# Performance work log

Hardware: AMD Instinct MI355X
Metric: run time of the kernel (lower is better)

The kernel has to match this reference:

```python
import jax, jax.numpy as jnp
import numpy as np

TANH_CLIP = 10.0
TEMP = 1.0


def setup_inputs() -> dict:
    key = jax.random.key(0)
    ks = jax.random.split(key, 8)
    B, N, E, H, SC = 1024, 1000, 128, 8, 256
    dk = E // H
    context = jax.random.normal(ks[0], (B, 1, E), dtype=jnp.float32)
    step_context = jax.random.normal(ks[1], (B, 1, SC), dtype=jnp.float32)
    # scale weights so tanh/softmax stay in a sane numeric range
    W_step = jax.random.normal(ks[2], (E, SC), dtype=jnp.float32) * 0.05
    glimpse_K = jax.random.normal(ks[3], (H, B, 1, N, dk), dtype=jnp.float32)
    glimpse_V = jax.random.normal(ks[4], (H, B, 1, N, dk), dtype=jnp.float32)
    logit_K = jax.random.normal(ks[5], (B, 1, N, E), dtype=jnp.float32)
    W_out = jax.random.normal(ks[6], (E, E), dtype=jnp.float32) * 0.05
    mask = jax.random.randint(ks[7], (B, 1, N), 0, 2).astype(bool)
    mask = mask.at[:, :, 0].set(False)  # guarantee at least one feasible node
    return {"context": context, "step_context": step_context, "W_step": W_step,
            "glimpse_K": glimpse_K, "glimpse_V": glimpse_V, "logit_K": logit_K,
            "W_out": W_out, "mask": mask}


def reference(context, step_context, W_step, glimpse_K, glimpse_V, logit_K, W_out, mask):
    B, S, E = context.shape          # S = num_steps = 1
    H = glimpse_K.shape[0]
    dk = E // H
    neg_inf = jnp.float32(-jnp.inf)
    # query = context_node_projected + project_step_context(step_context)
    query = context + jnp.einsum('bsc,ec->bse', step_context, W_step)  # [B,S,E]
    # split heads: glimpse_Q -> [H,B,S,dk] (the singleton q-dim of the torch code is folded)
    Q = query.reshape(B, S, H, dk).transpose(2, 0, 1, 3)
    # compatibility [H,B,S,N]
    compat = jnp.einsum('hbsk,hbsnk->hbsn', Q, glimpse_K) / jnp.sqrt(jnp.float32(dk))
    compat = jnp.where(mask[None], neg_inf, compat)       # mask_inner
    attn = jax.nn.softmax(compat, axis=-1)
    heads = jnp.einsum('hbsn,hbsnk->hbsk', attn, glimpse_V)  # [H,B,S,dk]
    glimpse = heads.transpose(1, 2, 0, 3).reshape(B, S, E)   # concat heads
    glimpse = jnp.einsum('bse,oe->bso', glimpse, W_out)      # project_out
    # logits against logit_K  [B,S,N]
    logits = jnp.einsum('bse,bsne->bsn', glimpse, logit_K) / jnp.sqrt(jnp.float32(E))
    logits = jnp.tanh(logits) * jnp.float32(TANH_CLIP)       # tanh clipping
    logits = jnp.where(mask, neg_inf, logits)                # mask_logits
    log_p = jax.nn.log_softmax(logits / jnp.float32(TEMP), axis=-1)
    return log_p
```

## Files before the change

### kernel.cpp

```cpp
#include <hip/hip_runtime.h>
#include <hip/hip_bf16.h>
#include <math.h>

#define NB  1024
#define NN  1000
#define NE  128
#define NH  8
#define NDK 16
#define NSC 256

typedef __attribute__((ext_vector_type(4))) float f32x4;

__device__ __forceinline__ f32x4 ld4(const float* p) {
    return *reinterpret_cast<const f32x4*>(p);
}

__global__ __launch_bounds__(512, 4)
void fused_kernel(const float* __restrict__ ctx, const float* __restrict__ stepc,
                  const float* __restrict__ Wstep,
                  const float* __restrict__ gK, const float* __restrict__ gV,
                  const float* __restrict__ lK, const float* __restrict__ Wout,
                  const unsigned char* __restrict__ mask,
                  __hip_bfloat16* __restrict__ out)
{
    const int b = blockIdx.x;
    const int t = threadIdx.x;
    const int w = t >> 6, lane = t & 63;
    const int qq  = lane & 3;
    const int rsl = lane >> 2;

    __shared__ __align__(16) float q_lds[NE];
    __shared__ float wmax[2][8], wsum[2][8];
    __shared__ __align__(16) float wred[2][8][16];
    __shared__ __align__(16) float g[NE];
    __shared__ __align__(16) float gout[NE];
    __shared__ float red[8];
    __shared__ float Mv, LSv;

    const unsigned int* mw = reinterpret_cast<const unsigned int*>(mask);
    const bool m_i32 = (__ballot(mw[lane] <= 1u) == ~0ull);
    const int* mask_i = reinterpret_cast<const int*>(mask);

    {
        const f32x4 sv = ld4(stepc + (size_t)b * NSC + lane * 4);
        #pragma unroll
        for (int r = 0; r < 16; ++r) {
            const int row = w * NDK + r;
            f32x4 wv = ld4(Wstep + (size_t)row * NSC + lane * 4);
            float p = wv.x * sv.x + wv.y * sv.y + wv.z * sv.z + wv.w * sv.w;
            #pragma unroll
            for (int off = 32; off > 0; off >>= 1) p += __shfl_xor(p, off);
            if (lane == 0) q_lds[row] = p + ctx[(size_t)b * NE + row];
        }
    }

    unsigned mbits = 0;
    #pragma unroll
    for (int i = 0; i < 8; ++i) {
        const int n = w * 16 + i * 128 + rsl;
        const bool dead = (n >= NN);
        const int nn = dead ? 0 : n;
        int mk = m_i32 ? (mask_i[(size_t)b * NN + nn] != 0)
                       : (mask[(size_t)b * NN + nn] != 0);
        mbits |= (unsigned)(mk | (dead ? 1 : 0)) << i;
    }
    __syncthreads();

    #pragma unroll 1
    for (int h = 0; h < NH; ++h) {
        const int pb = h & 1;
        const f32x4 qv = ld4(&q_lds[h * NDK + qq * 4]);
        const float* Kb = gK + (size_t)(h * NB + b) * NN * NDK;
        const float* Vb = gV + (size_t)(h * NB + b) * NN * NDK;

        f32x4 vreg[8];
        float sc[8];
        #pragma unroll
        for (int i = 0; i < 8; ++i) {
            const int n = w * 16 + i * 128 + rsl;
            const int nn = (n < NN) ? n : 0;
            const size_t off = (size_t)nn * NDK + qq * 4;
            f32x4 kv = ld4(Kb + off);
            vreg[i] = ld4(Vb + off);
            sc[i] = kv.x*qv.x + kv.y*qv.y + kv.z*qv.z + kv.w*qv.w;
        }
        #pragma unroll
        for (int i = 0; i < 8; ++i) {
            float p = sc[i];
            p += __shfl_xor(p, 1);
            p += __shfl_xor(p, 2);
            sc[i] = ((mbits >> i) & 1u) ? -INFINITY : p * 0.25f;
        }

        float m = sc[0];
        #pragma unroll
        for (int i = 1; i < 8; ++i) m = fmaxf(m, sc[i]);
        #pragma unroll
        for (int off = 32; off > 0; off >>= 1) m = fmaxf(m, __shfl_xor(m, off));
        if (lane == 0) wmax[pb][w] = m;
        __syncthreads();
        float M = wmax[pb][0];
        #pragma unroll
        for (int i = 1; i < 8; ++i) M = fmaxf(M, wmax[pb][i]);

        f32x4 acc = {0.f, 0.f, 0.f, 0.f};
        float ls = 0.f;
        #pragma unroll
        for (int i = 0; i < 8; ++i) {
            const float e = expf(sc[i] - M);
            ls += e;
            acc.x += e * vreg[i].x; acc.y += e * vreg[i].y;
            acc.z += e * vreg[i].z; acc.w += e * vreg[i].w;
        }
        #pragma unroll
        for (int off = 32; off > 0; off >>= 1) ls += __shfl_xor(ls, off);
        if (lane == 0) wsum[pb][w] = ls;

        #pragma unroll
        for (int off = 4; off < 64; off <<= 1) {
            acc.x += __shfl_xor(acc.x, off);
            acc.y += __shfl_xor(acc.y, off);
            acc.z += __shfl_xor(acc.z, off);
            acc.w += __shfl_xor(acc.w, off);
        }
        if (lane < 4) *reinterpret_cast<f32x4*>(&wred[pb][w][lane * 4]) = acc;
        __syncthreads();

        if (t < NDK) {
            float S = wsum[pb][0];
            #pragma unroll
            for (int i = 1; i < 8; ++i) S += wsum[pb][i];
            S *= 0.25f;
            float r = wred[pb][0][t];
            #pragma unroll
            for (int i = 1; i < 8; ++i) r += wred[pb][i][t];
            g[h * NDK + t] = r / S;
        }
    }
    __syncthreads();

    if (t < NE) {
        float a2 = 0.f;
        const float4* w4 = reinterpret_cast<const float4*>(Wout + (size_t)t * NE);
        const float4* g4 = reinterpret_cast<const float4*>(g);
        #pragma unroll 8
        for (int e4 = 0; e4 < NE / 4; ++e4) {
            float4 wv = w4[e4]; float4 gg = g4[e4];
            a2 += wv.x*gg.x + wv.y*gg.y + wv.z*gg.z + wv.w*gg.w;
        }
        gout[t] = a2;
    }
    __syncthreads();

    const f32x4* go4 = reinterpret_cast<const f32x4*>(gout);
    float lv[2];
    #pragma unroll
    for (int i = 0; i < 2; ++i) {
        const int n = t + 512 * i;
        const bool live = (n < NN);
        const int nidx = live ? n : 0;
        int mkd = m_i32 ? (mask_i[(size_t)b * NN + nidx] != 0)
                        : (mask[(size_t)b * NN + nidx] != 0);
        mkd |= (live ? 0 : 1);
        const int nn = mkd ? 0 : n;
        const float* lp = lK + ((size_t)b * NN + nn) * NE;
        float a3 = 0.f;
        #pragma unroll
        for (int c4 = 0; c4 < NE / 4; ++c4) {
            f32x4 x = ld4(lp + 4 * c4);
            f32x4 gv = go4[c4];
            a3 += x.x*gv.x + x.y*gv.y + x.z*gv.z + x.w*gv.w;
        }
        float val = tanhf(a3 * 0.08838834764831845f) * 10.0f;
        lv[i] = mkd ? -3.0e38f : val;
    }

    float mm = fmaxf(lv[0], lv[1]);
    #pragma unroll
    for (int off = 32; off > 0; off >>= 1) mm = fmaxf(mm, __shfl_xor(mm, off));
    if (lane == 0) red[w] = mm;
    __syncthreads();
    if (t == 0) {
        float m2 = red[0];
        #pragma unroll
        for (int i = 1; i < 8; ++i) m2 = fmaxf(m2, red[i]);
        Mv = m2;
    }
    __syncthreads();
    const float M2 = Mv;
    float s2 = expf(lv[0] - M2) + expf(lv[1] - M2);
    #pragma unroll
    for (int off = 32; off > 0; off >>= 1) s2 += __shfl_xor(s2, off);
    if (lane == 0) red[w] = s2;
    __syncthreads();
    if (t == 0) {
        float ss = 0.f;
        #pragma unroll
        for (int i = 0; i < 8; ++i) ss += red[i];
        LSv = M2 + logf(ss);
    }
    __syncthreads();
    const float LS = LSv;
    #pragma unroll
    for (int i = 0; i < 2; ++i) {
        const int n = t + 512 * i;
        if (n < NN)
            out[(size_t)b * NN + n] = __float2bfloat16(lv[i] - LS);
    }
}

extern "C" void kernel_launch(void* const* d_in, const int* in_sizes, int n_in,
                              void* d_out, int out_size, void* d_ws, size_t ws_size,
                              hipStream_t stream) {
    const float* ctx   = (const float*)d_in[0];
    const float* stepc = (const float*)d_in[1];
    const float* Wstep = (const float*)d_in[2];
    const float* gK    = (const float*)d_in[3];
    const float* gV    = (const float*)d_in[4];
    const float* lK    = (const float*)d_in[5];
    const float* Wout  = (const float*)d_in[6];
    const unsigned char* mask = (const unsigned char*)d_in[7];
    __hip_bfloat16* out = (__hip_bfloat16*)d_out;

    fused_kernel<<<dim3(NB), dim3(512), 0, stream>>>(
        ctx, stepc, Wstep, gK, gV, lK, Wout, mask, out);
}
```

Baseline: 257.5 us.

## Assign one head per wave with online softmax over nodes

Each of the 8 waves now owns one attention head and streams all 1000 nodes itself, keeping a running max, sum and accumulator (online softmax) instead of splitting nodes across waves with per-head block barriers. The query slice is computed straight into registers, so the LDS staging and the two __syncthreads per head go away. Masked nodes are redirected to row 0 so their K/V loads hit a single cached line, and fast __expf replaces expf. In exchange each wave runs a long serial loop with a rescale step per node, and the K/V loads inside one wave are less spread across memory.

```diff
diff --git a/kernel.cpp b/kernel.cpp
--- a/kernel.cpp
+++ b/kernel.cpp
@@ -8,6 +8,7 @@
 #define NH  8
 #define NDK 16
 #define NSC 256
+#define NIT 63
 
 typedef __attribute__((ext_vector_type(4))) float f32x4;
 
@@ -29,9 +30,6 @@
     const int qq  = lane & 3;
     const int rsl = lane >> 2;
 
-    __shared__ __align__(16) float q_lds[NE];
-    __shared__ float wmax[2][8], wsum[2][8];
-    __shared__ __align__(16) float wred[2][8][16];
     __shared__ __align__(16) float g[NE];
     __shared__ __align__(16) float gout[NE];
     __shared__ float red[8];
@@ -41,101 +39,78 @@
     const bool m_i32 = (__ballot(mw[lane] <= 1u) == ~0ull);
     const int* mask_i = reinterpret_cast<const int*>(mask);
 
+    float qv0 = 0.f, qv1 = 0.f, qv2 = 0.f, qv3 = 0.f;
     {
         const f32x4 sv = ld4(stepc + (size_t)b * NSC + lane * 4);
         #pragma unroll
-        for (int r = 0; r < 16; ++r) {
-            const int row = w * NDK + r;
-            f32x4 wv = ld4(Wstep + (size_t)row * NSC + lane * 4);
-            float p = wv.x * sv.x + wv.y * sv.y + wv.z * sv.z + wv.w * sv.w;
+        for (int rr = 0; rr < 4; ++rr) {
             #pragma unroll
-            for (int off = 32; off > 0; off >>= 1) p += __shfl_xor(p, off);
-            if (lane == 0) q_lds[row] = p + ctx[(size_t)b * NE + row];
+            for (int c = 0; c < 4; ++c) {
+                const int row = w * NDK + rr * 4 + c;
+                f32x4 wv = ld4(Wstep + (size_t)row * NSC + lane * 4);
+                float p = wv.x*sv.x + wv.y*sv.y + wv.z*sv.z + wv.w*sv.w;
+                #pragma unroll
+                for (int off = 32; off > 0; off >>= 1) p += __shfl_xor(p, off);
+                const float val = p + ctx[(size_t)b * NE + row];
+                const bool sel = (qq == rr);
+                if      (c == 0) qv0 = sel ? val : qv0;
+                else if (c == 1) qv1 = sel ? val : qv1;
+                else if (c == 2) qv2 = sel ? val : qv2;
+                else             qv3 = sel ? val : qv3;
+            }
         }
     }
 
-    unsigned mbits = 0;
-    #pragma unroll
-    for (int i = 0; i < 8; ++i) {
-        const int n = w * 16 + i * 128 + rsl;
+    const float* Kb = gK + (size_t)(w * NB + b) * NN * NDK;
+    const float* Vb = gV + (size_t)(w * NB + b) * NN * NDK;
+    float m = -3.0e38f, ls = 0.f;
+    f32x4 acc = {0.f, 0.f, 0.f, 0.f};
+    #pragma unroll 4
+    for (int it = 0; it < NIT; ++it) {
+        const int n = it * 16 + rsl;
         const bool dead = (n >= NN);
-        const int nn = dead ? 0 : n;
-        int mk = m_i32 ? (mask_i[(size_t)b * NN + nn] != 0)
-                       : (mask[(size_t)b * NN + nn] != 0);
-        mbits |= (unsigned)(mk | (dead ? 1 : 0)) << i;
-    }
-    __syncthreads();
-
-    #pragma unroll 1
-    for (int h = 0; h < NH; ++h) {
-        const int pb = h & 1;
-        const f32x4 qv = ld4(&q_lds[h * NDK + qq * 4]);
-        const float* Kb = gK + (size_t)(h * NB + b) * NN * NDK;
-        const float* Vb = gV + (size_t)(h * NB + b) * NN * NDK;
-
-        f32x4 vreg[8];
-        float sc[8];
-        #pragma unroll
-        for (int i = 0; i < 8; ++i) {
-            const int n = w * 16 + i * 128 + rsl;
-            const int nn = (n < NN) ? n : 0;
-            const size_t off = (size_t)nn * NDK + qq * 4;
-            f32x4 kv = ld4(Kb + off);
-            vreg[i] = ld4(Vb + off);
-            sc[i] = kv.x*qv.x + kv.y*qv.y + kv.z*qv.z + kv.w*qv.w;
-        }
-        #pragma unroll
-        for (int i = 0; i < 8; ++i) {
-            float p = sc[i];
-            p += __shfl_xor(p, 1);
-            p += __shfl_xor(p, 2);
-            sc[i] = ((mbits >> i) & 1u) ? -INFINITY : p * 0.25f;
-        }
-
-        float m = sc[0];
-        #pragma unroll
-        for (int i = 1; i < 8; ++i) m = fmaxf(m, sc[i]);
-        #pragma unroll
-        for (int off = 32; off > 0; off >>= 1) m = fmaxf(m, __shfl_xor(m, off));
-        if (lane == 0) wmax[pb][w] = m;
-        __syncthreads();
-        float M = wmax[pb][0];
-        #pragma unroll
-        for (int i = 1; i < 8; ++i) M = fmaxf(M, wmax[pb][i]);
-
-        f32x4 acc = {0.f, 0.f, 0.f, 0.f};
-        float ls = 0.f;
-        #pragma unroll
-        for (int i = 0; i < 8; ++i) {
-            const float e = expf(sc[i] - M);
-            ls += e;
-            acc.x += e * vreg[i].x; acc.y += e * vreg[i].y;
-            acc.z += e * vreg[i].z; acc.w += e * vreg[i].w;
-        }
-        #pragma unroll
-        for (int off = 32; off > 0; off >>= 1) ls += __shfl_xor(ls, off);
-        if (lane == 0) wsum[pb][w] = ls;
-
-        #pragma unroll
-        for (int off = 4; off < 64; off <<= 1) {
-            acc.x += __shfl_xor(acc.x, off);
-            acc.y += __shfl_xor(acc.y, off);
-            acc.z += __shfl_xor(acc.z, off);
-            acc.w += __shfl_xor(acc.w, off);
-        }
-        if (lane < 4) *reinterpret_cast<f32x4*>(&wred[pb][w][lane * 4]) = acc;
-        __syncthreads();
-
-        if (t < NDK) {
-            float S = wsum[pb][0];
-            #pragma unroll
-            for (int i = 1; i < 8; ++i) S += wsum[pb][i];
-            S *= 0.25f;
-            float r = wred[pb][0][t];
-            #pragma unroll
-            for (int i = 1; i < 8; ++i) r += wred[pb][i][t];
-            g[h * NDK + t] = r / S;
-        }
+        const int nm = dead ? 0 : n;
+        bool mk = m_i32 ? (mask_i[(size_t)b * NN + nm] != 0)
+                        : (mask[(size_t)b * NN + nm] != 0);
+        mk |= dead;
+        const int nn = mk ? 0 : n;
+        const size_t off = (size_t)nn * NDK + qq * 4;
+        f32x4 kv = ld4(Kb + off);
+        f32x4 vv = ld4(Vb + off);
+        float p = kv.x*qv0 + kv.y*qv1 + kv.z*qv2 + kv.w*qv3;
+        p += __shfl_xor(p, 1);
+        p += __shfl_xor(p, 2);
+        const float s = mk ? -INFINITY : p * 0.25f;
+        const float mn = fmaxf(m, s);
+        const float corr = __expf(m - mn);
+        const float e    = __expf(s - mn);
+        ls = ls * corr + e;
+        acc.x = acc.x * corr + e * vv.x;
+        acc.y = acc.y * corr + e * vv.y;
+        acc.z = acc.z * corr + e * vv.z;
+        acc.w = acc.w * corr + e * vv.w;
+        m = mn;
+    }
+
+    float M = m;
+    #pragma unroll
+    for (int off = 32; off > 0; off >>= 1) M = fmaxf(M, __shfl_xor(M, off));
+    const float sc = __expf(m - M);
+    ls *= sc;
+    acc.x *= sc; acc.y *= sc; acc.z *= sc; acc.w *= sc;
+    #pragma unroll
+    for (int off = 32; off > 0; off >>= 1) ls += __shfl_xor(ls, off);
+    #pragma unroll
+    for (int off = 4; off < 64; off <<= 1) {
+        acc.x += __shfl_xor(acc.x, off);
+        acc.y += __shfl_xor(acc.y, off);
+        acc.z += __shfl_xor(acc.z, off);
+        acc.w += __shfl_xor(acc.w, off);
+    }
+    if (rsl == 0) {
+        const float r = 4.0f / ls;
+        f32x4 gg = { acc.x * r, acc.y * r, acc.z * r, acc.w * r };
+        *reinterpret_cast<f32x4*>(&g[w * NDK + qq * 4]) = gg;
     }
     __syncthreads();
 
```

Measured after the change: 484.3 us. 88.1% more time.

## Split query projection into separate kernel and skip K/V loads for masked nodes

Applied to the files above, without the earlier changes.

Moves the step-context projection (query = ctx + stepc·Wstepᵀ) into a small prologue kernel that writes queries to the workspace, so the main kernel no longer does the per-block GEMV and its barrier before the attention loop. The main kernel reads q straight from global memory per head. It also redirects K/V loads for masked nodes to row 0, so those rows are not fetched and DRAM traffic on glimpse K/V drops by roughly half. The cost is an extra launch plus a workspace round trip, and the else branch uses the workspace even when it is too small.

```diff
diff --git a/kernel.cpp b/kernel.cpp
--- a/kernel.cpp
+++ b/kernel.cpp
@@ -15,9 +15,27 @@
     return *reinterpret_cast<const f32x4*>(p);
 }
 
+__global__ __launch_bounds__(128)
+void query_kernel(const float* __restrict__ ctx, const float* __restrict__ stepc,
+                  const float* __restrict__ Wstep, float* __restrict__ q_ws)
+{
+    const int b = blockIdx.x, t = threadIdx.x;
+    __shared__ float sc[NSC];
+    sc[t] = stepc[b * NSC + t];
+    sc[t + 128] = stepc[b * NSC + t + 128];
+    __syncthreads();
+    float acc = ctx[b * NE + t];
+    const float4* w4 = reinterpret_cast<const float4*>(Wstep + (size_t)t * NSC);
+    #pragma unroll 8
+    for (int c4 = 0; c4 < NSC / 4; ++c4) {
+        float4 w = w4[c4];
+        acc += sc[4*c4] * w.x + sc[4*c4+1] * w.y + sc[4*c4+2] * w.z + sc[4*c4+3] * w.w;
+    }
+    q_ws[b * NE + t] = acc;
+}
+
 __global__ __launch_bounds__(512, 4)
-void fused_kernel(const float* __restrict__ ctx, const float* __restrict__ stepc,
-                  const float* __restrict__ Wstep,
+void fused_kernel(const float* __restrict__ q_ws,
                   const float* __restrict__ gK, const float* __restrict__ gV,
                   const float* __restrict__ lK, const float* __restrict__ Wout,
                   const unsigned char* __restrict__ mask,
@@ -29,7 +47,6 @@
     const int qq  = lane & 3;
     const int rsl = lane >> 2;
 
-    __shared__ __align__(16) float q_lds[NE];
     __shared__ float wmax[2][8], wsum[2][8];
     __shared__ __align__(16) float wred[2][8][16];
     __shared__ __align__(16) float g[NE];
@@ -40,19 +57,6 @@
     const unsigned int* mw = reinterpret_cast<const unsigned int*>(mask);
     const bool m_i32 = (__ballot(mw[lane] <= 1u) == ~0ull);
     const int* mask_i = reinterpret_cast<const int*>(mask);
-
-    {
-        const f32x4 sv = ld4(stepc + (size_t)b * NSC + lane * 4);
-        #pragma unroll
-        for (int r = 0; r < 16; ++r) {
-            const int row = w * NDK + r;
-            f32x4 wv = ld4(Wstep + (size_t)row * NSC + lane * 4);
-            float p = wv.x * sv.x + wv.y * sv.y + wv.z * sv.z + wv.w * sv.w;
-            #pragma unroll
-            for (int off = 32; off > 0; off >>= 1) p += __shfl_xor(p, off);
-            if (lane == 0) q_lds[row] = p + ctx[(size_t)b * NE + row];
-        }
-    }
 
     unsigned mbits = 0;
     #pragma unroll
@@ -64,12 +68,11 @@
                        : (mask[(size_t)b * NN + nn] != 0);
         mbits |= (unsigned)(mk | (dead ? 1 : 0)) << i;
     }
-    __syncthreads();
 
     #pragma unroll 1
     for (int h = 0; h < NH; ++h) {
         const int pb = h & 1;
-        const f32x4 qv = ld4(&q_lds[h * NDK + qq * 4]);
+        const f32x4 qv = ld4(q_ws + (size_t)b * NE + h * NDK + qq * 4);
         const float* Kb = gK + (size_t)(h * NB + b) * NN * NDK;
         const float* Vb = gV + (size_t)(h * NB + b) * NN * NDK;
 
@@ -78,7 +81,7 @@
         #pragma unroll
         for (int i = 0; i < 8; ++i) {
             const int n = w * 16 + i * 128 + rsl;
-            const int nn = (n < NN) ? n : 0;
+            const int nn = ((mbits >> i) & 1u) ? 0 : n;
             const size_t off = (size_t)nn * NDK + qq * 4;
             f32x4 kv = ld4(Kb + off);
             vreg[i] = ld4(Vb + off);
@@ -222,6 +225,13 @@
     const unsigned char* mask = (const unsigned char*)d_in[7];
     __hip_bfloat16* out = (__hip_bfloat16*)d_out;
 
-    fused_kernel<<<dim3(NB), dim3(512), 0, stream>>>(
-        ctx, stepc, Wstep, gK, gV, lK, Wout, mask, out);
-}
+    const size_t need = (size_t)NB * NE * 4;
+    if (ws_size >= need) {
+        float* q_ws = (float*)d_ws;
+        query_kernel<<<dim3(NB), dim3(128), 0, stream>>>(ctx, stepc, Wstep, q_ws);
+        fused_kernel<<<dim3(NB), dim3(512), 0, stream>>>(q_ws, gK, gV, lK, Wout, mask, out);
+    } else {
+        query_kernel<<<dim3(NB), dim3(128), 0, stream>>>(ctx, stepc, Wstep, (float*)d_ws);
+        fused_kernel<<<dim3(NB), dim3(512), 0, stream>>>((float*)d_ws, gK, gV, lK, Wout, mask, out);
+    }
+}
```

Result: faster. 219.9 us (-14.6%).
